# Optimization experiments

Hardware: AMD Instinct MI355X
Metric: run time of the kernel (lower is better)

## Reference

```python
import math
import jax, jax.numpy as jnp
import numpy as np

_GELU_C = math.sqrt(2.0 / math.pi)

def _gelu_tanh(x):
    return 0.5 * x * (1.0 + jnp.tanh(_GELU_C * (x + 0.044715 * x * x * x)))

def _l2_normalize(v, eps=1e-12):
    # matches F.normalize: v / max(||v||, eps)
    n = jnp.sqrt(jnp.sum(v * v, axis=-1, keepdims=True))
    return v / jnp.maximum(n, eps)

def setup_inputs() -> dict:
    key = jax.random.key(0)
    k1, k2, k3 = jax.random.split(key, 3)
    B, T, D = 8, 2048, 1024
    x = jax.random.normal(k1, (B, T, D), dtype=jnp.float32)
    # nn.Parameter initial values from the module
    log_alpha = jnp.asarray(math.log(math.exp(0.5) - 1.0), dtype=jnp.float32)
    log_sigma = jnp.asarray(math.log(1.0), dtype=jnp.float32)
    return {"x": x, "log_alpha": log_alpha, "log_sigma": log_sigma}

def reference(x, log_alpha, log_sigma):
    B, T, D = x.shape
    alpha = jax.nn.softplus(log_alpha)
    sigma = jax.nn.softplus(log_sigma)
    scale = 1.0 / math.sqrt(D)
    # full strictly-past causal attention (triu with diagonal=0 masks self too)
    sim = jnp.einsum('btd,bsd->bts', x, x) * scale            # [B,T,T]
    causal = jnp.triu(jnp.ones((T, T), dtype=bool), k=0)      # True = masked
    sim = jnp.where(causal[None], -jnp.inf, sim)
    # NaN-safe masked softmax: fully-masked rows (t=0) -> all zeros,
    # matching torch softmax + nan_to_num(nan=0.0)
    m = jnp.max(sim, axis=-1, keepdims=True)
    m_safe = jnp.where(jnp.isfinite(m), m, 0.0)
    e = jnp.exp(sim - m_safe)                                 # -inf -> 0
    denom = jnp.sum(e, axis=-1, keepdims=True)
    attn = jnp.where(denom > 0, e / jnp.where(denom > 0, denom, 1.0), 0.0)
    context = jnp.einsum('bts,bsd->btd', attn, x)             # [B,T,D]
    cos_sim = jnp.sum(_l2_normalize(x) * _l2_normalize(context), axis=-1)  # [B,T]
    novelty = jnp.clip(1.0 - cos_sim, 0.0, 2.0) / 2.0
    novelty = jnp.nan_to_num(novelty, nan=1.0)
    gate = 1.0 + alpha * jnp.tanh(sigma * novelty[..., None])
    return _gelu_tanh(x * gate)
```

## Files before the change

### kernel.cpp

```cpp
#include <hip/hip_runtime.h>
#include <math.h>

#define TN 2048
#define DN 1024

typedef __attribute__((ext_vector_type(8))) _Float16 half8;
typedef __attribute__((ext_vector_type(4))) _Float16 half4v;
typedef __attribute__((ext_vector_type(4))) float f32x4;

__device__ __forceinline__ f32x4 mfma16(half8 a, half8 b, f32x4 c) {
  return __builtin_amdgcn_mfma_f32_16x16x32_f16(a, b, c, 0, 0, 0);
}

#define BAR_LDS()  asm volatile("s_waitcnt lgkmcnt(0)\ns_barrier" ::: "memory")
#define WAITVM16() asm volatile("s_waitcnt vmcnt(16)" ::: "memory")
#define WAITVM0()  asm volatile("s_waitcnt vmcnt(0)" ::: "memory")

__device__ __forceinline__ int img_off(int key, int f) {
  const int kg = key >> 2;
  const int p  = ((kg & 1) << 2) | (kg >> 1);
  return (f >> 4) * 512 + p * 64 + (key & 3) * 16 + (f & 15);
}

__global__ __launch_bounds__(256) void convert_x(const float* __restrict__ x,
                                                 _Float16* __restrict__ w) {
  const long long gid = (long long)blockIdx.x * 256 + threadIdx.x;
  const long long e   = gid * 8;
  const int bt   = (int)(e >> 15);
  const int et   = (int)(e & 32767);
  const int f16b = et >> 9;
  const int p    = (et >> 6) & 7;
  const int row  = (et >> 4) & 3;
  const int col0 = et & 15;
  const int kg   = ((p & 3) << 1) | (p >> 2);
  const int key  = kg * 4 + row;
  const size_t xoff = ((size_t)bt * 32 + key) * DN + f16b * 16 + col0;
  float4 u0 = *(const float4*)(x + xoff);
  float4 u1 = *(const float4*)(x + xoff + 4);
  half8 h = {(_Float16)u0.x, (_Float16)u0.y, (_Float16)u0.z, (_Float16)u0.w,
             (_Float16)u1.x, (_Float16)u1.y, (_Float16)u1.z, (_Float16)u1.w};
  *(half8*)(w + e) = h;
}

#define ISSUE4(T, O0, O1, O2, O3)                                             \
  asm volatile("ds_read_b64_tr_b16 %0, %4 offset:" O0 "\n\t"                  \
               "ds_read_b64_tr_b16 %1, %4 offset:" O1 "\n\t"                  \
               "ds_read_b64_tr_b16 %2, %4 offset:" O2 "\n\t"                  \
               "ds_read_b64_tr_b16 %3, %4 offset:" O3                         \
               : "=&v"(T[0]), "=&v"(T[1]), "=&v"(T[2]), "=&v"(T[3])           \
               : "v"(ab));

#define MFMA4(T, CT0, CT1)                                                    \
  {                                                                           \
    half8 bf0 = __builtin_shufflevector(T[0], T[1], 0, 1, 2, 3, 4, 5, 6, 7);  \
    half8 bf1 = __builtin_shufflevector(T[2], T[3], 0, 1, 2, 3, 4, 5, 6, 7);  \
    oacc[0][CT0] = mfma16(a0, bf0, oacc[0][CT0]);                             \
    oacc[1][CT0] = mfma16(a1, bf0, oacc[1][CT0]);                             \
    oacc[0][CT1] = mfma16(a0, bf1, oacc[0][CT1]);                             \
    oacc[1][CT1] = mfma16(a1, bf1, oacc[1][CT1]);                             \
  }

template <bool WS>
__global__ __launch_bounds__(512)
void attn_gate(const float* __restrict__ x, const _Float16* __restrict__ wsx,
               const float* __restrict__ pla, const float* __restrict__ pls,
               float* __restrict__ out) {
  __shared__ _Float16 Kbuf[2][32768];
  __shared__ _Float16 SredB[8][32][56];
  __shared__ float l_s[32], gate_s[32];

  const int tid = threadIdx.x;
  const int w   = tid >> 6;
  const int l   = tid & 63;
  const int lr  = l & 15;
  const int lg  = l >> 4;
  const int kq  = w;
  const int h24 = (lg >> 1) * 24;
  const int c8  = (lg & 1) * 8;
  const int kb  = (lg >> 1) * 16 + c8;

  const int b  = blockIdx.x & 7;
  const int pr = blockIdx.x >> 3;

  const float alpha = log1pf(expf(pla[0]));
  const float sigma = log1pf(expf(pls[0]));

  const float* xb = x + (size_t)b * TN * DN;
  float*       ob = out + (size_t)b * TN * DN;

  const int kg0 = lr >> 2;
  const int bk0 = ((((kg0 & 1) << 2) | (kg0 >> 1)) << 6) + (lr & 3) * 16 + (lg & 1) * 8;
  const int kg1 = 4 + (lr >> 2);
  const int bk1 = ((((kg1 & 1) << 2) | (kg1 >> 1)) << 6) + (lr & 3) * 16 + (lg & 1) * 8;

  for (int hv = 0; hv < 2; ++hv) {
    const int qt    = hv ? (63 - pr) : pr;
    const int qbase = qt * 32;
    const int nkt   = qt + 1;

    auto STAGE = [&](int t) {
      if constexpr (WS) {
        const _Float16* tn = wsx + (size_t)(b * 64 + t) * 32768;
#pragma unroll
        for (int i = 0; i < 8; ++i)
          __builtin_amdgcn_global_load_lds(
              (const __attribute__((address_space(1))) void*)(tn + w * 4096 + i * 512 + l * 8),
              (__attribute__((address_space(3))) void*)(&Kbuf[t & 1][w * 4096 + i * 512]), 16, 0, 0);
      } else {
        const int skey = tid >> 4, sc = tid & 15;
        const float* kp = xb + (size_t)(t * 32 + skey) * DN + sc * 4;
#pragma unroll
        for (int j = 0; j < 16; ++j) {
          const int f = sc * 4 + 64 * j;
          float4 v = *(const float4*)(kp + 64 * j);
          half4v h = {(_Float16)v.x, (_Float16)v.y, (_Float16)v.z, (_Float16)v.w};
          *(half4v*)&Kbuf[t & 1][img_off(skey, f)] = h;
        }
      }
    };

    STAGE(0);
    if (nkt > 1) STAGE(1);

    half8 qf0[4], qf1[4];
    if constexpr (WS) {
      const _Float16* qtile = wsx + (size_t)(b * 64 + qt) * 32768;
      const int r0  = lr;
      const int g0  = r0 >> 2;
      const int qp0 = (((g0 & 1) << 2) | (g0 >> 1)) * 64 + (r0 & 3) * 16 + (lg & 1) * 8;
      const int r1  = 16 + lr;
      const int g1  = r1 >> 2;
      const int qp1 = (((g1 & 1) << 2) | (g1 >> 1)) * 64 + (r1 & 3) * 16 + (lg & 1) * 8;
#pragma unroll
      for (int s = 0; s < 4; ++s) {
        const int base = (kq * 8 + s * 2 + (lg >> 1)) * 512;
        qf0[s] = *(const half8*)&qtile[base + qp0];
        qf1[s] = *(const half8*)&qtile[base + qp1];
      }
    } else {
#pragma unroll
      for (int s = 0; s < 4; ++s) {
        const float* qp0 = xb + (size_t)(qbase + lr) * DN + kq * 128 + s * 32 + lg * 8;
        const float* qp1 = xb + (size_t)(qbase + 16 + lr) * DN + kq * 128 + s * 32 + lg * 8;
        float4 a = ((const float4*)qp0)[0];
        float4 c = ((const float4*)qp0)[1];
        half8 h0;
        h0[0]=(_Float16)a.x; h0[1]=(_Float16)a.y; h0[2]=(_Float16)a.z; h0[3]=(_Float16)a.w;
        h0[4]=(_Float16)c.x; h0[5]=(_Float16)c.y; h0[6]=(_Float16)c.z; h0[7]=(_Float16)c.w;
        qf0[s] = h0;
        a = ((const float4*)qp1)[0];
        c = ((const float4*)qp1)[1];
        half8 h1;
        h1[0]=(_Float16)a.x; h1[1]=(_Float16)a.y; h1[2]=(_Float16)a.z; h1[3]=(_Float16)a.w;
        h1[4]=(_Float16)c.x; h1[5]=(_Float16)c.y; h1[6]=(_Float16)c.z; h1[7]=(_Float16)c.w;
        qf1[s] = h1;
      }
    }

    f32x4 oacc[2][8];
#pragma unroll
    for (int rt = 0; rt < 2; ++rt)
#pragma unroll
      for (int ct = 0; ct < 8; ++ct)
        oacc[rt][ct] = f32x4{0.f, 0.f, 0.f, 0.f};

    float l0 = 0.0f, l1 = 0.0f;

    if constexpr (!WS) __syncthreads();

    for (int t = 0; t < nkt; ++t) {
      if constexpr (WS) {
        if (t + 1 < nkt) { WAITVM16(); } else { WAITVM0(); }
      }

      {
        f32x4 s00 = f32x4{0.f,0.f,0.f,0.f}, s01 = f32x4{0.f,0.f,0.f,0.f};
        f32x4 s10 = f32x4{0.f,0.f,0.f,0.f}, s11 = f32x4{0.f,0.f,0.f,0.f};
        const _Float16* kbp = &Kbuf[t & 1][0];
#pragma unroll
        for (int s = 0; s < 4; ++s) {
          const int base = (kq * 8 + s * 2 + (lg >> 1)) * 512;
          half8 bf0 = *(const half8*)&kbp[base + bk0];
          half8 bf1 = *(const half8*)&kbp[base + bk1];
          s00 = mfma16(qf0[s], bf0, s00);
          s10 = mfma16(qf1[s], bf0, s10);
          s01 = mfma16(qf0[s], bf1, s01);
          s11 = mfma16(qf1[s], bf1, s11);
        }
#pragma unroll
        for (int j = 0; j < 4; ++j) {
          SredB[kq][lg * 4 + j][lr]           = (_Float16)s00[j];
          SredB[kq][lg * 4 + j][24 + lr]      = (_Float16)s01[j];
          SredB[kq][16 + lg * 4 + j][lr]      = (_Float16)s10[j];
          SredB[kq][16 + lg * 4 + j][24 + lr] = (_Float16)s11[j];
        }
      }
      BAR_LDS();

      {
        half8 r00 = *(const half8*)&SredB[0][lr][h24 + c8];
        half8 r01 = *(const half8*)&SredB[1][lr][h24 + c8];
        half8 r02 = *(const half8*)&SredB[2][lr][h24 + c8];
        half8 r03 = *(const half8*)&SredB[3][lr][h24 + c8];
        half8 r04 = *(const half8*)&SredB[4][lr][h24 + c8];
        half8 r05 = *(const half8*)&SredB[5][lr][h24 + c8];
        half8 r06 = *(const half8*)&SredB[6][lr][h24 + c8];
        half8 r07 = *(const half8*)&SredB[7][lr][h24 + c8];
        half8 sum0 = ((r00 + r01) + (r02 + r03)) + ((r04 + r05) + (r06 + r07));
        half8 r10 = *(const half8*)&SredB[0][16 + lr][h24 + c8];
        half8 r11 = *(const half8*)&SredB[1][16 + lr][h24 + c8];
        half8 r12 = *(const half8*)&SredB[2][16 + lr][h24 + c8];
        half8 r13 = *(const half8*)&SredB[3][16 + lr][h24 + c8];
        half8 r14 = *(const half8*)&SredB[4][16 + lr][h24 + c8];
        half8 r15 = *(const half8*)&SredB[5][16 + lr][h24 + c8];
        half8 r16 = *(const half8*)&SredB[6][16 + lr][h24 + c8];
        half8 r17 = *(const half8*)&SredB[7][16 + lr][h24 + c8];
        half8 sum1 = ((r10 + r11) + (r12 + r13)) + ((r14 + r15) + (r16 + r17));

        const bool mt = (t == nkt - 1);
        half8 a0, a1;
#pragma unroll
        for (int j = 0; j < 8; ++j) {
          float p0 = __expf((float)sum0[j] * 0.03125f);
          float p1 = __expf((float)sum1[j] * 0.03125f);
          if (mt) {
            if (kb + j >= lr)      p0 = 0.0f;
            if (kb + j >= 16 + lr) p1 = 0.0f;
          }
          l0 += p0; l1 += p1;
          a0[j] = (_Float16)p0;
          a1[j] = (_Float16)p1;
        }

        const uint32_t ab = (uint32_t)(uintptr_t)(void*)&Kbuf[t & 1][w * 4096 + l * 4];
        asm volatile("s_waitcnt lgkmcnt(0)" ::: "memory");
        __builtin_amdgcn_sched_barrier(0);
        half4v t0[4], t1[4];
        ISSUE4(t0, "0", "512", "1024", "1536");
        ISSUE4(t1, "2048", "2560", "3072", "3584");
        asm volatile("s_waitcnt lgkmcnt(4)" ::: "memory");
        __builtin_amdgcn_sched_barrier(0);
        MFMA4(t0, 0, 1);
        ISSUE4(t0, "4096", "4608", "5120", "5632");
        asm volatile("s_waitcnt lgkmcnt(4)" ::: "memory");
        __builtin_amdgcn_sched_barrier(0);
        MFMA4(t1, 2, 3);
        ISSUE4(t1, "6144", "6656", "7168", "7680");
        asm volatile("s_waitcnt lgkmcnt(4)" ::: "memory");
        __builtin_amdgcn_sched_barrier(0);
        MFMA4(t0, 4, 5);
        asm volatile("s_waitcnt lgkmcnt(0)" ::: "memory");
        __builtin_amdgcn_sched_barrier(0);
        MFMA4(t1, 6, 7);
      }
      BAR_LDS();

      if (t + 2 < nkt) {
        STAGE(t + 2);
        if constexpr (!WS) __syncthreads();
      }
    }

    {
      float lt0 = l0 + __shfl_xor(l0, 16); lt0 += __shfl_xor(lt0, 32);
      float lt1 = l1 + __shfl_xor(l1, 16); lt1 += __shfl_xor(lt1, 32);
      if (w == 0 && lg == 0) { l_s[lr] = lt0; l_s[16 + lr] = lt1; }
    }

    {
      float* ered = (float*)&SredB[0][0][0];
#pragma unroll
      for (int rt = 0; rt < 2; ++rt)
#pragma unroll
        for (int j = 0; j < 4; ++j) {
          const int row = rt * 16 + lg * 4 + j;
          const float* xr = xb + (size_t)(qbase + row) * DN + w * 128 + lr;
          float a1 = 0.f, a2 = 0.f, a3 = 0.f;
#pragma unroll
          for (int ct = 0; ct < 8; ++ct) {
            const float xv = xr[ct * 16];
            const float ov = oacc[rt][ct][j];
            a1 += xv * ov; a2 += xv * xv; a3 += ov * ov;
          }
#pragma unroll
          for (int d = 1; d < 16; d <<= 1) {
            a1 += __shfl_xor(a1, d);
            a2 += __shfl_xor(a2, d);
            a3 += __shfl_xor(a3, d);
          }
          if (lr == 0) {
            float* e = ered + (row * 8 + w) * 4;
            e[0] = a1; e[1] = a2; e[2] = a3;
          }
        }
    }
    __syncthreads();
    if (tid < 32) {
      const float* ered = (const float*)&SredB[0][0][0];
      float SxO = 0.f, Sxx = 0.f, SOO = 0.f;
#pragma unroll
      for (int wv = 0; wv < 8; ++wv) {
        const float* e = ered + (tid * 8 + wv) * 4;
        SxO += e[0]; Sxx += e[1]; SOO += e[2];
      }
      const float lden = l_s[tid];
      float cosv = 0.0f;
      if (lden > 0.0f) {
        const float nx = fmaxf(sqrtf(Sxx), 1e-12f);
        const float nc = fmaxf(sqrtf(SOO) / lden, 1e-12f);
        cosv = (SxO / lden) / (nx * nc);
      }
      float nov = fminf(fmaxf(1.0f - cosv, 0.0f), 2.0f) * 0.5f;
      gate_s[tid] = 1.0f + alpha * tanhf(sigma * nov);
    }
    __syncthreads();
    {
#pragma unroll
      for (int rt = 0; rt < 2; ++rt)
#pragma unroll
        for (int j = 0; j < 4; ++j) {
          const int row = rt * 16 + lg * 4 + j;
          const float g = gate_s[row];
          const float* xr = xb + (size_t)(qbase + row) * DN + w * 128 + lr;
          float* orow     = ob + (size_t)(qbase + row) * DN + w * 128 + lr;
#pragma unroll
          for (int ct = 0; ct < 8; ++ct) {
            const float z = xr[ct * 16] * g;
            const float u = 0.7978845608028654f * (z + 0.044715f * z * z * z);
            orow[ct * 16] = 0.5f * z * (1.0f + tanhf(u));
          }
        }
    }
    __syncthreads();
  }
}

extern "C" void kernel_launch(void* const* d_in, const int* in_sizes, int n_in,
                              void* d_out, int out_size, void* d_ws, size_t ws_size,
                              hipStream_t stream) {
  const float* x  = (const float*)d_in[0];
  const float* la = (const float*)d_in[1];
  const float* ls = (const float*)d_in[2];
  float* out = (float*)d_out;
  const size_t need = (size_t)8 * 64 * 32768 * 2;
  if (ws_size >= need) {
    convert_x<<<dim3(8192), dim3(256), 0, stream>>>(x, (_Float16*)d_ws);
    attn_gate<true><<<dim3(256), dim3(512), 0, stream>>>(
        x, (const _Float16*)d_ws, la, ls, out);
  } else {
    attn_gate<false><<<dim3(256), dim3(512), 0, stream>>>(
        x, (const _Float16*)nullptr, la, ls, out);
  }
}
```

Measured before the change: 217.6 us.

## Split attention into 16-row query blocks with single-buffered K and more CTAs

Replaces the 256 blocks, each handling two paired 32-row query tiles with double-buffered K tiles, by 1024 blocks that each handle one 16-row query tile. K is single-buffered with a full wait before each tile, which shrinks LDS so that four blocks can share a CU (launch_bounds 512,4). Blocks are ordered longest-first to help load balance. The goal is higher occupancy and finer work distribution. The cost is that K/V tiles are re-read twice as often across blocks, and the load of the next tile no longer overlaps compute within a block.

```diff
diff --git a/kernel.cpp b/kernel.cpp
--- a/kernel.cpp
+++ b/kernel.cpp
@@ -13,7 +13,6 @@
 }
 
 #define BAR_LDS()  asm volatile("s_waitcnt lgkmcnt(0)\ns_barrier" ::: "memory")
-#define WAITVM16() asm volatile("s_waitcnt vmcnt(16)" ::: "memory")
 #define WAITVM0()  asm volatile("s_waitcnt vmcnt(0)" ::: "memory")
 
 __device__ __forceinline__ int img_off(int key, int f) {
@@ -50,24 +49,22 @@
                : "=&v"(T[0]), "=&v"(T[1]), "=&v"(T[2]), "=&v"(T[3])           \
                : "v"(ab));
 
-#define MFMA4(T, CT0, CT1)                                                    \
+#define MFMA2(T, CT0, CT1)                                                    \
   {                                                                           \
     half8 bf0 = __builtin_shufflevector(T[0], T[1], 0, 1, 2, 3, 4, 5, 6, 7);  \
     half8 bf1 = __builtin_shufflevector(T[2], T[3], 0, 1, 2, 3, 4, 5, 6, 7);  \
-    oacc[0][CT0] = mfma16(a0, bf0, oacc[0][CT0]);                             \
-    oacc[1][CT0] = mfma16(a1, bf0, oacc[1][CT0]);                             \
-    oacc[0][CT1] = mfma16(a0, bf1, oacc[0][CT1]);                             \
-    oacc[1][CT1] = mfma16(a1, bf1, oacc[1][CT1]);                             \
+    oacc[CT0] = mfma16(aP, bf0, oacc[CT0]);                                   \
+    oacc[CT1] = mfma16(aP, bf1, oacc[CT1]);                                   \
   }
 
 template <bool WS>
-__global__ __launch_bounds__(512)
+__global__ __launch_bounds__(512, 4)
 void attn_gate(const float* __restrict__ x, const _Float16* __restrict__ wsx,
                const float* __restrict__ pla, const float* __restrict__ pls,
                float* __restrict__ out) {
-  __shared__ _Float16 Kbuf[2][32768];
-  __shared__ _Float16 SredB[8][32][56];
-  __shared__ float l_s[32], gate_s[32];
+  __shared__ _Float16 Kbuf[32768];
+  __shared__ _Float16 Sred[8][16][40];
+  __shared__ float l_s[16], gate_s[16];
 
   const int tid = threadIdx.x;
   const int w   = tid >> 6;
@@ -75,12 +72,11 @@
   const int lr  = l & 15;
   const int lg  = l >> 4;
   const int kq  = w;
-  const int h24 = (lg >> 1) * 24;
-  const int c8  = (lg & 1) * 8;
-  const int kb  = (lg >> 1) * 16 + c8;
-
-  const int b  = blockIdx.x & 7;
-  const int pr = blockIdx.x >> 3;
+
+  const int b   = blockIdx.x & 7;
+  const int q16 = 127 - (blockIdx.x >> 3);
+  const int qbase = q16 * 16;
+  const int nkt   = (qbase + 14) / 32 + 1;
 
   const float alpha = log1pf(expf(pla[0]));
   const float sigma = log1pf(expf(pls[0]));
@@ -93,245 +89,195 @@
   const int kg1 = 4 + (lr >> 2);
   const int bk1 = ((((kg1 & 1) << 2) | (kg1 >> 1)) << 6) + (lr & 3) * 16 + (lg & 1) * 8;
 
-  for (int hv = 0; hv < 2; ++hv) {
-    const int qt    = hv ? (63 - pr) : pr;
-    const int qbase = qt * 32;
-    const int nkt   = qt + 1;
-
-    auto STAGE = [&](int t) {
-      if constexpr (WS) {
-        const _Float16* tn = wsx + (size_t)(b * 64 + t) * 32768;
-#pragma unroll
-        for (int i = 0; i < 8; ++i)
-          __builtin_amdgcn_global_load_lds(
-              (const __attribute__((address_space(1))) void*)(tn + w * 4096 + i * 512 + l * 8),
-              (__attribute__((address_space(3))) void*)(&Kbuf[t & 1][w * 4096 + i * 512]), 16, 0, 0);
-      } else {
-        const int skey = tid >> 4, sc = tid & 15;
-        const float* kp = xb + (size_t)(t * 32 + skey) * DN + sc * 4;
-#pragma unroll
-        for (int j = 0; j < 16; ++j) {
-          const int f = sc * 4 + 64 * j;
-          float4 v = *(const float4*)(kp + 64 * j);
-          half4v h = {(_Float16)v.x, (_Float16)v.y, (_Float16)v.z, (_Float16)v.w};
-          *(half4v*)&Kbuf[t & 1][img_off(skey, f)] = h;
-        }
-      }
-    };
-
-    STAGE(0);
-    if (nkt > 1) STAGE(1);
-
-    half8 qf0[4], qf1[4];
+  auto STAGE = [&](int t) {
     if constexpr (WS) {
-      const _Float16* qtile = wsx + (size_t)(b * 64 + qt) * 32768;
-      const int r0  = lr;
-      const int g0  = r0 >> 2;
-      const int qp0 = (((g0 & 1) << 2) | (g0 >> 1)) * 64 + (r0 & 3) * 16 + (lg & 1) * 8;
-      const int r1  = 16 + lr;
-      const int g1  = r1 >> 2;
-      const int qp1 = (((g1 & 1) << 2) | (g1 >> 1)) * 64 + (r1 & 3) * 16 + (lg & 1) * 8;
+      const _Float16* tn = wsx + (size_t)(b * 64 + t) * 32768;
+#pragma unroll
+      for (int i = 0; i < 8; ++i)
+        __builtin_amdgcn_global_load_lds(
+            (const __attribute__((address_space(1))) void*)(tn + w * 4096 + i * 512 + l * 8),
+            (__attribute__((address_space(3))) void*)(&Kbuf[w * 4096 + i * 512]), 16, 0, 0);
+    } else {
+      const int skey = tid >> 4, sc = tid & 15;
+      const float* kp = xb + (size_t)(t * 32 + skey) * DN + sc * 4;
+#pragma unroll
+      for (int j = 0; j < 16; ++j) {
+        const int f = sc * 4 + 64 * j;
+        float4 v = *(const float4*)(kp + 64 * j);
+        half4v h = {(_Float16)v.x, (_Float16)v.y, (_Float16)v.z, (_Float16)v.w};
+        *(half4v*)&Kbuf[img_off(skey, f)] = h;
+      }
+    }
+  };
+
+  STAGE(0);
+
+  half8 qf[4];
+  if constexpr (WS) {
+    const _Float16* qtile = wsx + (size_t)(b * 64 + (q16 >> 1)) * 32768;
+    const int qrow = (q16 & 1) * 16 + lr;
+    const int g0   = qrow >> 2;
+    const int qp   = (((g0 & 1) << 2) | (g0 >> 1)) * 64 + (qrow & 3) * 16 + (lg & 1) * 8;
+#pragma unroll
+    for (int s = 0; s < 4; ++s)
+      qf[s] = *(const half8*)&qtile[(kq * 8 + s * 2 + (lg >> 1)) * 512 + qp];
+  } else {
+#pragma unroll
+    for (int s = 0; s < 4; ++s) {
+      const float* qp = xb + (size_t)(qbase + lr) * DN + kq * 128 + s * 32 + lg * 8;
+      float4 a = ((const float4*)qp)[0];
+      float4 c = ((const float4*)qp)[1];
+      half8 h;
+      h[0]=(_Float16)a.x; h[1]=(_Float16)a.y; h[2]=(_Float16)a.z; h[3]=(_Float16)a.w;
+      h[4]=(_Float16)c.x; h[5]=(_Float16)c.y; h[6]=(_Float16)c.z; h[7]=(_Float16)c.w;
+      qf[s] = h;
+    }
+  }
+
+  f32x4 oacc[8];
+#pragma unroll
+  for (int ct = 0; ct < 8; ++ct) oacc[ct] = f32x4{0.f, 0.f, 0.f, 0.f};
+  float l0 = 0.0f;
+
+  if constexpr (!WS) __syncthreads();
+
+  for (int t = 0; t < nkt; ++t) {
+    if constexpr (WS) WAITVM0();
+
+    {
+      f32x4 sA = f32x4{0.f,0.f,0.f,0.f};
+      f32x4 sB = f32x4{0.f,0.f,0.f,0.f};
 #pragma unroll
       for (int s = 0; s < 4; ++s) {
         const int base = (kq * 8 + s * 2 + (lg >> 1)) * 512;
-        qf0[s] = *(const half8*)&qtile[base + qp0];
-        qf1[s] = *(const half8*)&qtile[base + qp1];
-      }
-    } else {
-#pragma unroll
-      for (int s = 0; s < 4; ++s) {
-        const float* qp0 = xb + (size_t)(qbase + lr) * DN + kq * 128 + s * 32 + lg * 8;
-        const float* qp1 = xb + (size_t)(qbase + 16 + lr) * DN + kq * 128 + s * 32 + lg * 8;
-        float4 a = ((const float4*)qp0)[0];
-        float4 c = ((const float4*)qp0)[1];
-        half8 h0;
-        h0[0]=(_Float16)a.x; h0[1]=(_Float16)a.y; h0[2]=(_Float16)a.z; h0[3]=(_Float16)a.w;
-        h0[4]=(_Float16)c.x; h0[5]=(_Float16)c.y; h0[6]=(_Float16)c.z; h0[7]=(_Float16)c.w;
-        qf0[s] = h0;
-        a = ((const float4*)qp1)[0];
-        c = ((const float4*)qp1)[1];
-        half8 h1;
-        h1[0]=(_Float16)a.x; h1[1]=(_Float16)a.y; h1[2]=(_Float16)a.z; h1[3]=(_Float16)a.w;
-        h1[4]=(_Float16)c.x; h1[5]=(_Float16)c.y; h1[6]=(_Float16)c.z; h1[7]=(_Float16)c.w;
-        qf1[s] = h1;
-      }
-    }
-
-    f32x4 oacc[2][8];
-#pragma unroll
-    for (int rt = 0; rt < 2; ++rt)
-#pragma unroll
-      for (int ct = 0; ct < 8; ++ct)
-        oacc[rt][ct] = f32x4{0.f, 0.f, 0.f, 0.f};
-
-    float l0 = 0.0f, l1 = 0.0f;
-
-    if constexpr (!WS) __syncthreads();
-
-    for (int t = 0; t < nkt; ++t) {
-      if constexpr (WS) {
-        if (t + 1 < nkt) { WAITVM16(); } else { WAITVM0(); }
-      }
-
-      {
-        f32x4 s00 = f32x4{0.f,0.f,0.f,0.f}, s01 = f32x4{0.f,0.f,0.f,0.f};
-        f32x4 s10 = f32x4{0.f,0.f,0.f,0.f}, s11 = f32x4{0.f,0.f,0.f,0.f};
-        const _Float16* kbp = &Kbuf[t & 1][0];
-#pragma unroll
-        for (int s = 0; s < 4; ++s) {
-          const int base = (kq * 8 + s * 2 + (lg >> 1)) * 512;
-          half8 bf0 = *(const half8*)&kbp[base + bk0];
-          half8 bf1 = *(const half8*)&kbp[base + bk1];
-          s00 = mfma16(qf0[s], bf0, s00);
-          s10 = mfma16(qf1[s], bf0, s10);
-          s01 = mfma16(qf0[s], bf1, s01);
-          s11 = mfma16(qf1[s], bf1, s11);
-        }
-#pragma unroll
-        for (int j = 0; j < 4; ++j) {
-          SredB[kq][lg * 4 + j][lr]           = (_Float16)s00[j];
-          SredB[kq][lg * 4 + j][24 + lr]      = (_Float16)s01[j];
-          SredB[kq][16 + lg * 4 + j][lr]      = (_Float16)s10[j];
-          SredB[kq][16 + lg * 4 + j][24 + lr] = (_Float16)s11[j];
-        }
-      }
-      BAR_LDS();
-
-      {
-        half8 r00 = *(const half8*)&SredB[0][lr][h24 + c8];
-        half8 r01 = *(const half8*)&SredB[1][lr][h24 + c8];
-        half8 r02 = *(const half8*)&SredB[2][lr][h24 + c8];
-        half8 r03 = *(const half8*)&SredB[3][lr][h24 + c8];
-        half8 r04 = *(const half8*)&SredB[4][lr][h24 + c8];
-        half8 r05 = *(const half8*)&SredB[5][lr][h24 + c8];
-        half8 r06 = *(const half8*)&SredB[6][lr][h24 + c8];
-        half8 r07 = *(const half8*)&SredB[7][lr][h24 + c8];
-        half8 sum0 = ((r00 + r01) + (r02 + r03)) + ((r04 + r05) + (r06 + r07));
-        half8 r10 = *(const half8*)&SredB[0][16 + lr][h24 + c8];
-        half8 r11 = *(const half8*)&SredB[1][16 + lr][h24 + c8];
-        half8 r12 = *(const half8*)&SredB[2][16 + lr][h24 + c8];
-        half8 r13 = *(const half8*)&SredB[3][16 + lr][h24 + c8];
-        half8 r14 = *(const half8*)&SredB[4][16 + lr][h24 + c8];
-        half8 r15 = *(const half8*)&SredB[5][16 + lr][h24 + c8];
-        half8 r16 = *(const half8*)&SredB[6][16 + lr][h24 + c8];
-        half8 r17 = *(const half8*)&SredB[7][16 + lr][h24 + c8];
-        half8 sum1 = ((r10 + r11) + (r12 + r13)) + ((r14 + r15) + (r16 + r17));
-
-        const bool mt = (t == nkt - 1);
-        half8 a0, a1;
-#pragma unroll
-        for (int j = 0; j < 8; ++j) {
-          float p0 = __expf((float)sum0[j] * 0.03125f);
-          float p1 = __expf((float)sum1[j] * 0.03125f);
-          if (mt) {
-            if (kb + j >= lr)      p0 = 0.0f;
-            if (kb + j >= 16 + lr) p1 = 0.0f;
-          }
-          l0 += p0; l1 += p1;
-          a0[j] = (_Float16)p0;
-          a1[j] = (_Float16)p1;
-        }
-
-        const uint32_t ab = (uint32_t)(uintptr_t)(void*)&Kbuf[t & 1][w * 4096 + l * 4];
-        asm volatile("s_waitcnt lgkmcnt(0)" ::: "memory");
-        __builtin_amdgcn_sched_barrier(0);
-        half4v t0[4], t1[4];
-        ISSUE4(t0, "0", "512", "1024", "1536");
-        ISSUE4(t1, "2048", "2560", "3072", "3584");
-        asm volatile("s_waitcnt lgkmcnt(4)" ::: "memory");
-        __builtin_amdgcn_sched_barrier(0);
-        MFMA4(t0, 0, 1);
-        ISSUE4(t0, "4096", "4608", "5120", "5632");
-        asm volatile("s_waitcnt lgkmcnt(4)" ::: "memory");
-        __builtin_amdgcn_sched_barrier(0);
-        MFMA4(t1, 2, 3);
-        ISSUE4(t1, "6144", "6656", "7168", "7680");
-        asm volatile("s_waitcnt lgkmcnt(4)" ::: "memory");
-        __builtin_amdgcn_sched_barrier(0);
-        MFMA4(t0, 4, 5);
-        asm volatile("s_waitcnt lgkmcnt(0)" ::: "memory");
-        __builtin_amdgcn_sched_barrier(0);
-        MFMA4(t1, 6, 7);
-      }
-      BAR_LDS();
-
-      if (t + 2 < nkt) {
-        STAGE(t + 2);
-        if constexpr (!WS) __syncthreads();
-      }
-    }
+        half8 bf0 = *(const half8*)&Kbuf[base + bk0];
+        half8 bf1 = *(const half8*)&Kbuf[base + bk1];
+        sA = mfma16(bf0, qf[s], sA);
+        sB = mfma16(bf1, qf[s], sB);
+      }
+      half4v hA = {(_Float16)sA[0], (_Float16)sA[1], (_Float16)sA[2], (_Float16)sA[3]};
+      half4v hB = {(_Float16)sB[0], (_Float16)sB[1], (_Float16)sB[2], (_Float16)sB[3]};
+      *(half4v*)&Sred[kq][lr][lg * 4]      = hA;
+      *(half4v*)&Sred[kq][lr][16 + lg * 4] = hB;
+    }
+    BAR_LDS();
 
     {
-      float lt0 = l0 + __shfl_xor(l0, 16); lt0 += __shfl_xor(lt0, 32);
-      float lt1 = l1 + __shfl_xor(l1, 16); lt1 += __shfl_xor(lt1, 32);
-      if (w == 0 && lg == 0) { l_s[lr] = lt0; l_s[16 + lr] = lt1; }
-    }
-
-    {
-      float* ered = (float*)&SredB[0][0][0];
-#pragma unroll
-      for (int rt = 0; rt < 2; ++rt)
-#pragma unroll
-        for (int j = 0; j < 4; ++j) {
-          const int row = rt * 16 + lg * 4 + j;
-          const float* xr = xb + (size_t)(qbase + row) * DN + w * 128 + lr;
-          float a1 = 0.f, a2 = 0.f, a3 = 0.f;
-#pragma unroll
-          for (int ct = 0; ct < 8; ++ct) {
-            const float xv = xr[ct * 16];
-            const float ov = oacc[rt][ct][j];
-            a1 += xv * ov; a2 += xv * xv; a3 += ov * ov;
-          }
-#pragma unroll
-          for (int d = 1; d < 16; d <<= 1) {
-            a1 += __shfl_xor(a1, d);
-            a2 += __shfl_xor(a2, d);
-            a3 += __shfl_xor(a3, d);
-          }
-          if (lr == 0) {
-            float* e = ered + (row * 8 + w) * 4;
-            e[0] = a1; e[1] = a2; e[2] = a3;
-          }
-        }
-    }
-    __syncthreads();
-    if (tid < 32) {
-      const float* ered = (const float*)&SredB[0][0][0];
-      float SxO = 0.f, Sxx = 0.f, SOO = 0.f;
-#pragma unroll
-      for (int wv = 0; wv < 8; ++wv) {
-        const float* e = ered + (tid * 8 + wv) * 4;
-        SxO += e[0]; Sxx += e[1]; SOO += e[2];
-      }
-      const float lden = l_s[tid];
-      float cosv = 0.0f;
-      if (lden > 0.0f) {
-        const float nx = fmaxf(sqrtf(Sxx), 1e-12f);
-        const float nc = fmaxf(sqrtf(SOO) / lden, 1e-12f);
-        cosv = (SxO / lden) / (nx * nc);
-      }
-      float nov = fminf(fmaxf(1.0f - cosv, 0.0f), 2.0f) * 0.5f;
-      gate_s[tid] = 1.0f + alpha * tanhf(sigma * nov);
-    }
-    __syncthreads();
-    {
-#pragma unroll
-      for (int rt = 0; rt < 2; ++rt)
-#pragma unroll
-        for (int j = 0; j < 4; ++j) {
-          const int row = rt * 16 + lg * 4 + j;
-          const float g = gate_s[row];
-          const float* xr = xb + (size_t)(qbase + row) * DN + w * 128 + lr;
-          float* orow     = ob + (size_t)(qbase + row) * DN + w * 128 + lr;
-#pragma unroll
-          for (int ct = 0; ct < 8; ++ct) {
-            const float z = xr[ct * 16] * g;
-            const float u = 0.7978845608028654f * (z + 0.044715f * z * z * z);
-            orow[ct * 16] = 0.5f * z * (1.0f + tanhf(u));
-          }
-        }
-    }
-    __syncthreads();
+      half8 r0 = *(const half8*)&Sred[0][lr][lg * 8];
+      half8 r1 = *(const half8*)&Sred[1][lr][lg * 8];
+      half8 r2 = *(const half8*)&Sred[2][lr][lg * 8];
+      half8 r3 = *(const half8*)&Sred[3][lr][lg * 8];
+      half8 r4 = *(const half8*)&Sred[4][lr][lg * 8];
+      half8 r5 = *(const half8*)&Sred[5][lr][lg * 8];
+      half8 r6 = *(const half8*)&Sred[6][lr][lg * 8];
+      half8 r7 = *(const half8*)&Sred[7][lr][lg * 8];
+      half8 sum = ((r0 + r1) + (r2 + r3)) + ((r4 + r5) + (r6 + r7));
+
+      const bool mt = (t == nkt - 1);
+      const int  gb = 32 * t + lg * 8;
+      half8 aP;
+#pragma unroll
+      for (int j = 0; j < 8; ++j) {
+        float p = __expf((float)sum[j] * 0.03125f);
+        if (mt && (gb + j >= qbase + lr)) p = 0.0f;
+        l0 += p;
+        aP[j] = (_Float16)p;
+      }
+
+      const uint32_t ab = (uint32_t)(uintptr_t)(void*)&Kbuf[w * 4096 + l * 4];
+      asm volatile("s_waitcnt lgkmcnt(0)" ::: "memory");
+      __builtin_amdgcn_sched_barrier(0);
+      half4v t0[4], t1[4];
+      ISSUE4(t0, "0", "512", "1024", "1536");
+      ISSUE4(t1, "2048", "2560", "3072", "3584");
+      asm volatile("s_waitcnt lgkmcnt(4)" ::: "memory");
+      __builtin_amdgcn_sched_barrier(0);
+      MFMA2(t0, 0, 1);
+      ISSUE4(t0, "4096", "4608", "5120", "5632");
+      asm volatile("s_waitcnt lgkmcnt(4)" ::: "memory");
+      __builtin_amdgcn_sched_barrier(0);
+      MFMA2(t1, 2, 3);
+      ISSUE4(t1, "6144", "6656", "7168", "7680");
+      asm volatile("s_waitcnt lgkmcnt(4)" ::: "memory");
+      __builtin_amdgcn_sched_barrier(0);
+      MFMA2(t0, 4, 5);
+      asm volatile("s_waitcnt lgkmcnt(0)" ::: "memory");
+      __builtin_amdgcn_sched_barrier(0);
+      MFMA2(t1, 6, 7);
+    }
+
+    if (t + 1 < nkt) {
+      if constexpr (!WS) __syncthreads();
+      STAGE(t + 1);
+    }
+    BAR_LDS();
+  }
+
+  {
+    float lt = l0 + __shfl_xor(l0, 16);
+    lt += __shfl_xor(lt, 32);
+    if (w == 0 && lg == 0) l_s[lr] = lt;
+  }
+
+  {
+    float* ered = (float*)&Sred[0][0][0];
+#pragma unroll
+    for (int j = 0; j < 4; ++j) {
+      const int row = lg * 4 + j;
+      const float* xr = xb + (size_t)(qbase + row) * DN + w * 128 + lr;
+      float a1 = 0.f, a2 = 0.f, a3 = 0.f;
+#pragma unroll
+      for (int ct = 0; ct < 8; ++ct) {
+        const float xv = xr[ct * 16];
+        const float ov = oacc[ct][j];
+        a1 += xv * ov; a2 += xv * xv; a3 += ov * ov;
+      }
+#pragma unroll
+      for (int d = 1; d < 16; d <<= 1) {
+        a1 += __shfl_xor(a1, d);
+        a2 += __shfl_xor(a2, d);
+        a3 += __shfl_xor(a3, d);
+      }
+      if (lr == 0) {
+        float* e = ered + (row * 8 + w) * 4;
+        e[0] = a1; e[1] = a2; e[2] = a3;
+      }
+    }
+  }
+  __syncthreads();
+  if (tid < 16) {
+    const float* ered = (const float*)&Sred[0][0][0];
+    float SxO = 0.f, Sxx = 0.f, SOO = 0.f;
+#pragma unroll
+    for (int wv = 0; wv < 8; ++wv) {
+      const float* e = ered + (tid * 8 + wv) * 4;
+      SxO += e[0]; Sxx += e[1]; SOO += e[2];
+    }
+    const float lden = l_s[tid];
+    float cosv = 0.0f;
+    if (lden > 0.0f) {
+      const float nx = fmaxf(sqrtf(Sxx), 1e-12f);
+      const float nc = fmaxf(sqrtf(SOO) / lden, 1e-12f);
+      cosv = (SxO / lden) / (nx * nc);
+    }
+    float nov = fminf(fmaxf(1.0f - cosv, 0.0f), 2.0f) * 0.5f;
+    gate_s[tid] = 1.0f + alpha * tanhf(sigma * nov);
+  }
+  __syncthreads();
+  {
+#pragma unroll
+    for (int j = 0; j < 4; ++j) {
+      const int row = lg * 4 + j;
+      const float g = gate_s[row];
+      const float* xr = xb + (size_t)(qbase + row) * DN + w * 128 + lr;
+      float* orow     = ob + (size_t)(qbase + row) * DN + w * 128 + lr;
+#pragma unroll
+      for (int ct = 0; ct < 8; ++ct) {
+        const float z = xr[ct * 16] * g;
+        const float u = 0.7978845608028654f * (z + 0.044715f * z * z * z);
+        orow[ct * 16] = 0.5f * z * (1.0f + tanhf(u));
+      }
+    }
   }
 }
 
@@ -345,10 +291,10 @@
   const size_t need = (size_t)8 * 64 * 32768 * 2;
   if (ws_size >= need) {
     convert_x<<<dim3(8192), dim3(256), 0, stream>>>(x, (_Float16*)d_ws);
-    attn_gate<true><<<dim3(256), dim3(512), 0, stream>>>(
+    attn_gate<true><<<dim3(1024), dim3(512), 0, stream>>>(
         x, (const _Float16*)d_ws, la, ls, out);
   } else {
-    attn_gate<false><<<dim3(256), dim3(512), 0, stream>>>(
+    attn_gate<false><<<dim3(1024), dim3(512), 0, stream>>>(
         x, (const _Float16*)nullptr, la, ls, out);
   }
 }
```

Result: faster. 194.8 us (-10.5%).
